# Performance work log

Hardware: AMD Instinct MI355X
Metric: run time of the kernel (lower is better)

## Reference

```python
import jax, jax.numpy as jnp
import numpy as np

B, L, D = 32, 512, 128          # batch, seq_len, d_model (= num graph nodes N)
E, HS, DTR, U = 64, 64, 4, 32   # d_proj_E, d_proj_H (state), dt_rank, d_proj_U
R, K, DE, NH = 3, 3, 10, 4      # mamba layers, cheb order, d_e, heads
EPS = 1e-5


def _ln(x, g, b):
    m = jnp.mean(x, -1, keepdims=True)
    v = jnp.mean((x - m) ** 2, -1, keepdims=True)
    return (x - m) / jnp.sqrt(v + EPS) * g + b


def _mamba(x, in_w, conv_w, conv_b, xproj_w, dt_w, dt_b, Alog, Dp, out_w):
    b, l, _ = x.shape
    xz = x @ in_w                                  # (b,l,2E)
    xp, res = xz[..., :E], xz[..., E:]
    xc = jnp.transpose(xp, (0, 2, 1))              # (b,E,l)
    # causal depthwise conv: torch pads both sides by d_conv-1 then slices [:l]
    xc = jax.lax.conv_general_dilated(
        xc, conv_w, (1,), [(conv_w.shape[-1] - 1, 0)],
        dimension_numbers=('NCH', 'OIH', 'NCH'), feature_group_count=E)
    xc = xc + conv_b[None, :, None]
    xp = jax.nn.silu(jnp.transpose(xc, (0, 2, 1)))  # (b,l,E)
    xdbl = xp @ xproj_w                             # (b,l,DTR+2*HS)
    delta = jax.nn.softplus(xdbl[..., :DTR] @ dt_w + dt_b)        # (b,l,E)
    Bm = xdbl[..., DTR:DTR + HS]                                   # (b,l,HS)
    Cm = xdbl[..., DTR + HS:]                                      # (b,l,HS)
    A = -jnp.exp(Alog)                                             # (E,HS)
    dA = jnp.exp(delta[..., None] * A)                             # (b,l,E,HS)
    dBu = delta[..., None] * Bm[:, :, None, :] * xp[..., None]     # (b,l,E,HS)

    def step(s, t):
        dA_t, dBu_t, C_t = t
        s = dA_t * s + dBu_t
        return s, jnp.einsum('bdn,bn->bd', s, C_t)

    _, ys = jax.lax.scan(step, jnp.zeros((b, E, HS), x.dtype),
                         (jnp.swapaxes(dA, 0, 1), jnp.swapaxes(dBu, 0, 1),
                          jnp.swapaxes(Cm, 0, 1)))
    y = jnp.swapaxes(ys, 0, 1) + xp * Dp
    y = y * jax.nn.sigmoid(res)
    return y @ out_w


def _forward(x, mb_in_w, mb_conv_w, mb_conv_b, mb_xproj_w, mb_dt_w, mb_dt_b,
             mb_Alog, mb_D, mb_out_w, ln1_g, ln1_b, ln2_g, ln2_b,
             ffn_w1, ffn_b1, ffn_w2, ffn_b2,
             psi_emb, psi, W_q, W_k, attn_alpha, F_w, f_b, head_mix,
             head_w, head_b):
    # ---- bidirectional Mamba stack ----
    for i in range(R):
        f, bk = 2 * i, 2 * i + 1
        Y1 = _mamba(x, mb_in_w[f], mb_conv_w[f], mb_conv_b[f], mb_xproj_w[f],
                    mb_dt_w[f], mb_dt_b[f], mb_Alog[f], mb_D[f], mb_out_w[f])
        Y2 = jnp.flip(_mamba(jnp.flip(x, 1), mb_in_w[bk], mb_conv_w[bk],
                             mb_conv_b[bk], mb_xproj_w[bk], mb_dt_w[bk],
                             mb_dt_b[bk], mb_Alog[bk], mb_D[bk], mb_out_w[bk]), 1)
        Y3 = _ln(x + Y1 + Y2, ln1_g[i], ln1_b[i])
        Yp = jax.nn.relu(Y3 @ ffn_w1[i] + ffn_b1[i]) @ ffn_w2[i] + ffn_b2[i]
        x = _ln(Yp + Y3, ln2_g[i], ln2_b[i])
    h = jnp.transpose(x, (0, 2, 1))                # (B, N=D, L)
    # ---- MAGAC (deterministic single MC sample, eval, no edge drop) ----
    diff = psi_emb[:, None, :] - psi_emb[None, :, :]
    A_g = jax.nn.softmax(jnp.exp(-psi * jnp.sum(diff * diff, -1)), axis=1)
    Q = jnp.einsum('nd,dhm->nhm', psi_emb, W_q)
    Kt = jnp.einsum('nd,dhm->nhm', psi_emb, W_k)
    attn = jax.nn.softmax(jnp.einsum('nhd,mhd->hnm', Q, Kt)
                          / jnp.sqrt(jnp.asarray(DE, x.dtype)), axis=-1)
    alpha = jax.nn.sigmoid(attn_alpha)
    A_effs = alpha * A_g[None] + (1.0 - alpha) * attn   # (H,N,N)
    mix = jax.nn.softmax(head_mix)
    I = jnp.eye(D, dtype=x.dtype)
    out = jnp.zeros((x.shape[0], D), x.dtype)
    for hh in range(NH):
        A = A_effs[hh]
        sup = [I, A]
        for _ in range(2, K + 1):
            sup.append(2.0 * A @ sup[-1] - sup[-2])
        S = jnp.stack(sup, 0)                             # (K+1,N,N)
        Wf = jnp.einsum('nd,dkl->nkl', psi_emb, F_w[hh])  # (N,K+1,L)
        bf = psi_emb @ f_b[hh]                            # (N,)
        out_h = jnp.einsum('knm,bml,nkl->bn', S, h, Wf) + bf
        out = out + mix[hh] * out_h
    log_var = jnp.zeros_like(out)
    pred = out @ head_w + head_b                          # (B,1)
    return pred, log_var


def setup_inputs() -> dict:
    key = jax.random.key(0)
    ks = iter(jax.random.split(key, 40))
    nrm = lambda shp, s=0.05: (jax.random.normal(next(ks), shp, jnp.float32) * s)
    M = 2 * R
    base_Alog = jnp.log(jnp.arange(1, HS + 1, dtype=jnp.float32))
    inp = {
        'x': jax.random.normal(next(ks), (B, L, D), jnp.float32),
        'mb_in_w': nrm((M, D, 2 * E)),
        'mb_conv_w': nrm((M, E, 1, 3), 0.2),
        'mb_conv_b': jnp.zeros((M, E), jnp.float32),
        'mb_xproj_w': nrm((M, E, DTR + 2 * HS)),
        'mb_dt_w': nrm((M, DTR, E), 0.2),
        'mb_dt_b': jnp.zeros((M, E), jnp.float32),
        'mb_Alog': jnp.tile(base_Alog[None, None, :], (M, E, 1)),
        'mb_D': jnp.ones((M, E), jnp.float32),
        'mb_out_w': nrm((M, E, D)),
        'ln1_g': jnp.ones((R, D), jnp.float32),
        'ln1_b': jnp.zeros((R, D), jnp.float32),
        'ln2_g': jnp.ones((R, D), jnp.float32),
        'ln2_b': jnp.zeros((R, D), jnp.float32),
        'ffn_w1': nrm((R, D, U)),
        'ffn_b1': jnp.zeros((R, U), jnp.float32),
        'ffn_w2': nrm((R, U, D)),
        'ffn_b2': jnp.zeros((R, D), jnp.float32),
        'psi_emb': jax.random.normal(next(ks), (D, DE), jnp.float32),
        'psi': jnp.asarray(1.0, jnp.float32),
        'W_q': jax.random.normal(next(ks), (DE, NH, DE), jnp.float32),
        'W_k': jax.random.normal(next(ks), (DE, NH, DE), jnp.float32),
        'attn_alpha': jnp.asarray(0.5, jnp.float32),
        'F_w': nrm((NH, DE, K + 1, L), 0.05),
        'f_b': nrm((NH, DE), 1.0),
        'head_mix': jnp.ones((NH,), jnp.float32),
        'head_w': nrm((D, 1)),
        'head_b': jnp.zeros((1,), jnp.float32),
    }
    return inp


def reference(x, mb_in_w, mb_conv_w, mb_conv_b, mb_xproj_w, mb_dt_w, mb_dt_b,
              mb_Alog, mb_D, mb_out_w, ln1_g, ln1_b, ln2_g, ln2_b,
              ffn_w1, ffn_b1, ffn_w2, ffn_b2,
              psi_emb, psi, W_q, W_k, attn_alpha, F_w, f_b, head_mix,
              head_w, head_b):
    return _forward(x, mb_in_w, mb_conv_w, mb_conv_b, mb_xproj_w, mb_dt_w,
                    mb_dt_b, mb_Alog, mb_D, mb_out_w, ln1_g, ln1_b, ln2_g,
                    ln2_b, ffn_w1, ffn_b1, ffn_w2, ffn_b2, psi_emb, psi,
                    W_q, W_k, attn_alpha, F_w, f_b, head_mix, head_w, head_b)
```

## Files before the change

### kernel.cpp

```cpp
#include <hip/hip_runtime.h>
#include <hip/hip_bf16.h>


#define B_ 32
#define L_ 512
#define D_ 128
#define E_ 64
#define HS_ 64

#define OFF_X     0u
#define OFF_XZF   2097152u
#define OFF_XZB   4194304u
#define OFF_XPF   6291456u
#define OFF_XPB   7340032u
#define OFF_PKF   8388608u
#define OFF_PKB   10485760u
#define OFF_XBCF  12582912u
#define OFF_XBCB  14680064u
#define OFF_YSF   16777216u
#define OFF_YSB   17825792u
#define OFF_V     2097152u
#define OFF_WFT   10485760u
#define OFF_STT   11534336u
#define OFF_AEFF  11796480u
#define OFF_PART  12582912u
#define OFF_RED1  16777216u

__device__ __forceinline__ float sigf(float x) { return 1.f / (1.f + __expf(-x)); }
__device__ __forceinline__ unsigned int bf16r(float x) {
    unsigned int u = __float_as_uint(x);
    return (u + 0x7fffu + ((u >> 16) & 1u)) >> 16;
}

__global__ __launch_bounds__(256) void gemm_in2_kernel(
    const float* __restrict__ X, const float* __restrict__ WF, const float* __restrict__ WB,
    float* __restrict__ xzF, float* __restrict__ xzB)
{
    __shared__ float sxT[128][36];
    __shared__ float sw[2][16][128];
    const int tid = threadIdx.x;
    const int r0 = blockIdx.x * 32;
    for (int q = tid; q < 1024; q += 256) {
        const int r = q >> 5, k4 = q & 31;
        const float4 v = *(const float4*)&X[(size_t)(r0 + r) * 128 + k4 * 4];
        sxT[k4 * 4 + 0][r] = v.x; sxT[k4 * 4 + 1][r] = v.y;
        sxT[k4 * 4 + 2][r] = v.z; sxT[k4 * 4 + 3][r] = v.w;
    }
    const int wv = tid >> 6, lane = tid & 63;
    const int d = wv >> 1, ch = wv & 1;
    const int r4 = lane >> 4, c16 = lane & 15;
    float4 acc[8];
#pragma unroll
    for (int j = 0; j < 8; ++j) acc[j] = float4{0.f, 0.f, 0.f, 0.f};
    for (int ko = 0; ko < 128; ko += 16) {
        __syncthreads();
        for (int q = tid; q < 1024; q += 256) {
            const int dd = q >> 9, kk = (q >> 5) & 15, c4 = q & 31;
            *(float4*)&sw[dd][kk][c4 * 4] =
                *(const float4*)&((dd ? WB : WF)[(ko + kk) * 128 + c4 * 4]);
        }
        __syncthreads();
#pragma unroll
        for (int kk = 0; kk < 16; ++kk) {
            const float4 w4 = *(const float4*)&sw[d][kk][ch * 64 + c16 * 4];
            const float4 xa = *(const float4*)&sxT[ko + kk][r4 * 8];
            const float4 xb = *(const float4*)&sxT[ko + kk][r4 * 8 + 4];
            const float xs[8] = {xa.x, xa.y, xa.z, xa.w, xb.x, xb.y, xb.z, xb.w};
#pragma unroll
            for (int j = 0; j < 8; ++j) {
                acc[j].x = fmaf(xs[j], w4.x, acc[j].x);
                acc[j].y = fmaf(xs[j], w4.y, acc[j].y);
                acc[j].z = fmaf(xs[j], w4.z, acc[j].z);
                acc[j].w = fmaf(xs[j], w4.w, acc[j].w);
            }
        }
    }
    float* xz = d ? xzB : xzF;
#pragma unroll
    for (int j = 0; j < 8; ++j) {
        *(float4*)&xz[(r0 + r4 * 8 + j) * 128 + ch * 64 + c16 * 4] = acc[j];
    }
}

__global__ __launch_bounds__(256) void prep4_kernel(
    const float* __restrict__ xzF_, const float* __restrict__ xzB_,
    const float* __restrict__ conv_w, const float* __restrict__ conv_b,
    const float* __restrict__ xproj_w, const float* __restrict__ dt_w,
    const float* __restrict__ dt_b, int layer,
    float* __restrict__ xpF_, float* __restrict__ xpB_,
    unsigned int* __restrict__ xbcF_, unsigned int* __restrict__ xbcB_,
    float* __restrict__ pkF_, float* __restrict__ pkB_)
{
    __shared__ float sW[8448];
    __shared__ float sxp4[4][64][4];
    __shared__ float sdl4[4][4][4];
    const int tid = threadIdx.x, wv = tid >> 6, lane = tid & 63;
    const int dir = (int)(blockIdx.x >= 1024);
    const int r0 = (blockIdx.x & 1023) * 16;
    const int b = r0 >> 9;
    const int m = layer * 2 + dir;
    const float* Wg = xproj_w + m * 8448;
    for (int q = tid; q < 2112; q += 256) ((float4*)sW)[q] = ((const float4*)Wg)[q];
    const float* xz = dir ? xzB_ : xzF_;
    float* xp  = dir ? xpB_  : xpF_;
    unsigned int* xbc = dir ? xbcB_ : xbcF_;
    float* pkx = dir ? pkB_  : pkF_;
    const float* cw = conv_w + m * 192 + lane * 3;
    const float cw0 = cw[0], cw1 = cw[1], cw2 = cw[2];
    const float cb  = conv_b[m * 64 + lane];
    const float dtb = dt_b[m * 64 + lane];
    const float* dwp = dt_w + m * 256;
    const float dw0 = dwp[lane], dw1 = dwp[64 + lane], dw2 = dwp[128 + lane], dw3 = dwp[192 + lane];
    float uu[4];
#pragma unroll
    for (int it = 0; it < 4; ++it) {
        const int row = r0 + wv * 4 + it;
        const int l = row & 511;
        const int l1 = dir ? l + 1 : l - 1;
        const int l2 = dir ? l + 2 : l - 2;
        float acc = cb;
        const float x0 = xz[(size_t)row * 128 + lane];
        const float x1 = (l1 >= 0 && l1 < 512) ? xz[(size_t)(b * 512 + l1) * 128 + lane] : 0.f;
        const float x2 = (l2 >= 0 && l2 < 512) ? xz[(size_t)(b * 512 + l2) * 128 + lane] : 0.f;
        acc += cw0 * x2 + cw1 * x1 + cw2 * x0;
        const float u = acc * sigf(acc);
        xp[row * 64 + lane] = u;
        uu[it] = u;
    }
    *(float4*)&sxp4[wv][lane][0] = float4{uu[0], uu[1], uu[2], uu[3]};
    __syncthreads();
    const int jdt = lane & 3;
    float aB[4] = {0.f, 0.f, 0.f, 0.f};
    float aC[4] = {0.f, 0.f, 0.f, 0.f};
    float adt[4] = {0.f, 0.f, 0.f, 0.f};
#pragma unroll 4
    for (int k = 0; k < 64; ++k) {
        const float wB = sW[k * 132 + 4 + lane];
        const float wC = sW[k * 132 + 68 + lane];
        const float wd = sW[k * 132 + jdt];
        const float4 xv = *(const float4*)&sxp4[wv][k][0];
        aB[0] = fmaf(xv.x, wB, aB[0]); aC[0] = fmaf(xv.x, wC, aC[0]); adt[0] = fmaf(xv.x, wd, adt[0]);
        aB[1] = fmaf(xv.y, wB, aB[1]); aC[1] = fmaf(xv.y, wC, aC[1]); adt[1] = fmaf(xv.y, wd, adt[1]);
        aB[2] = fmaf(xv.z, wB, aB[2]); aC[2] = fmaf(xv.z, wC, aC[2]); adt[2] = fmaf(xv.z, wd, adt[2]);
        aB[3] = fmaf(xv.w, wB, aB[3]); aC[3] = fmaf(xv.w, wC, aC[3]); adt[3] = fmaf(xv.w, wd, adt[3]);
    }
#pragma unroll
    for (int it = 0; it < 4; ++it) {
        const int row = r0 + wv * 4 + it;
        xbc[row * 64 + lane] = (bf16r(aC[it]) << 16) | bf16r(aB[it]);
        if (lane < 4) sdl4[wv][it][lane] = adt[it];
    }
#pragma unroll
    for (int it = 0; it < 4; ++it) {
        const int row = r0 + wv * 4 + it;
        float dpre = fmaf(sdl4[wv][it][0], dw0, dtb);
        dpre = fmaf(sdl4[wv][it][1], dw1, dpre);
        dpre = fmaf(sdl4[wv][it][2], dw2, dpre);
        dpre = fmaf(sdl4[wv][it][3], dw3, dpre);
        const float dlt = (dpre > 20.f) ? dpre : log1pf(__expf(dpre));
        ((float2*)pkx)[row * 64 + lane] = float2{dlt, dlt * uu[it]};
    }
}

__global__ __launch_bounds__(256, 4) void scan8_kernel(
    const unsigned int* __restrict__ xbcF, const unsigned int* __restrict__ xbcB,
    const float* __restrict__ pkF, const float* __restrict__ pkB,
    const float* __restrict__ AlogF, const float* __restrict__ AlogB,
    float* __restrict__ ysF, float* __restrict__ ysB)
{
    __shared__ unsigned int sbc[2][1024];
    __shared__ float spk[2][4][16][2];
    __shared__ float ytile[4][16][68];
    const int tid = threadIdx.x, wv = tid >> 6, lane = tid & 63;
    const int bx = blockIdx.x;
    const int db = bx & 63;
    const int dir = db >> 5;
    const int b   = db & 31;
    const int e0  = (bx >> 6) * 4;
    const int e   = e0 + wv;
    const unsigned int* xbc = dir ? xbcB : xbcF;
    const float* pk  = dir ? pkB  : pkF;
    const float* Aw  = dir ? AlogB : AlogF;
    float* ys = dir ? ysB : ysF;
    const float a2 = -__expf(Aw[e * 64 + lane]) * 1.4426950408889634f;
    float s = 0.f;
    float* yrow = ys + (size_t)(b * 64 + e) * 512;

    const int psl = tid & 15, pw_ = tid >> 4;

#define STG_LOAD(RS)                                                              \
    {                                                                             \
        nb = *(const uint4*)(xbc + (size_t)(RS) * 64 + tid * 4);                  \
        if (tid < 64)                                                             \
            npp = *(const float2*)(pk + (size_t)((RS) + psl) * 128 + (e0 + pw_) * 2); \
    }
#define STG_WRITE(BUF)                                                            \
    {                                                                             \
        *(uint4*)(&sbc[BUF][tid * 4]) = nb;                                       \
        if (tid < 64) *(float2*)(&spk[BUF][pw_][psl][0]) = npp;                   \
    }

#define SCAN16(REV)                                                               \
    {                                                                             \
        const unsigned int* bc = &sbc[cur][0];                                    \
        const float* pq = &spk[cur][wv][0][0];                                    \
        _Pragma("unroll")                                                         \
        for (int j = 0; j < 8; ++j) {                                             \
            const int pj = (REV) ? 7 - j : j;                                     \
            const float4 pk4 = *(const float4*)(pq + pj * 4);                     \
            const int sA = (REV) ? 15 - 2 * j : 2 * j;                            \
            const int sB = (REV) ? 14 - 2 * j : 2 * j + 1;                        \
            const float dlA = (REV) ? pk4.z : pk4.x;                              \
            const float duA = (REV) ? pk4.w : pk4.y;                              \
            const float dlB = (REV) ? pk4.x : pk4.z;                              \
            const float duB = (REV) ? pk4.y : pk4.w;                              \
            const unsigned int bA = bc[sA * 64 + lane];                           \
            const float BnA = __uint_as_float(bA << 16);                          \
            const float CnA = __uint_as_float(bA & 0xffff0000u);                  \
            s = fmaf(__builtin_amdgcn_exp2f(dlA * a2), s, duA * BnA);             \
            ytile[wv][2 * j][lane] = s * CnA;                                     \
            const unsigned int bB = bc[sB * 64 + lane];                           \
            const float BnB = __uint_as_float(bB << 16);                          \
            const float CnB = __uint_as_float(bB & 0xffff0000u);                  \
            s = fmaf(__builtin_amdgcn_exp2f(dlB * a2), s, duB * BnB);             \
            ytile[wv][2 * j + 1][lane] = s * CnB;                                 \
        }                                                                         \
    }

    {
        uint4 nb; float2 npp;
        const int rs0 = b * 512 + (dir ? 496 : 0);
        STG_LOAD(rs0);
        STG_WRITE(0);
    }
    __syncthreads();

    int cur = 0;
    const int rr = lane & 15, sg = lane >> 4;
    for (int t = 0; t < 32; ++t) {
        uint4 nb; float2 npp;
        const bool more = (t + 1) < 32;
        if (more) {
            const int rs = b * 512 + (dir ? (496 - (t + 1) * 16) : ((t + 1) * 16));
            STG_LOAD(rs);
        }
        if (dir == 0) { SCAN16(0) } else { SCAN16(1) }
        {
            const float* yt = &ytile[wv][rr][sg * 16];
            const float4 A0 = *(const float4*)yt;
            const float4 A1 = *(const float4*)(yt + 4);
            const float4 A2 = *(const float4*)(yt + 8);
            const float4 A3 = *(const float4*)(yt + 12);
            float p = ((A0.x + A0.y) + (A0.z + A0.w)) + ((A1.x + A1.y) + (A1.z + A1.w))
                    + ((A2.x + A2.y) + (A2.z + A2.w)) + ((A3.x + A3.y) + (A3.z + A3.w));
            p += __shfl_xor(p, 16);
            p += __shfl_xor(p, 32);
            if (lane < 16) {
                const int lg = dir ? (511 - (t * 16 + rr)) : (t * 16 + rr);
                yrow[lg] = p;
            }
        }
        if (more) STG_WRITE(cur ^ 1);
        __syncthreads();
        cur ^= 1;
    }
#undef STG_LOAD
#undef STG_WRITE
#undef SCAN16
}

__global__ __launch_bounds__(256) void opfn2_kernel(
    const float* __restrict__ ysF, const float* __restrict__ ysB,
    const float* __restrict__ xpF, const float* __restrict__ xpB,
    const float* __restrict__ xzF, const float* __restrict__ xzB,
    const float* __restrict__ Dp, int layer,
    const float* __restrict__ Xc, const float* __restrict__ out_w,
    const float* __restrict__ W1, const float* __restrict__ b1,
    const float* __restrict__ W2, const float* __restrict__ b2,
    const float* __restrict__ g1, const float* __restrict__ bb1,
    const float* __restrict__ g2, const float* __restrict__ bb2,
    float* __restrict__ xout,
    const float* __restrict__ WFn, const float* __restrict__ WBn,
    float* __restrict__ xzFo, float* __restrict__ xzBo)
{
    __shared__ float smem[8832];
    float* syt = smem;
    float* y3  = smem;
    float* sy  = smem + 2176;
    float* sw  = smem + 4224;
    float* sh  = smem + 8320;
    const int tid = threadIdx.x;
    const int r0 = blockIdx.x * 16;
    const int b = r0 >> 9, l0 = r0 & 511;

    for (int q = tid; q < 512; q += 256) {
        const int d = q >> 8, ee = (q >> 2) & 63, rq = q & 3;
        const float* ysp = d ? ysB : ysF;
        const float4 v = *(const float4*)&ysp[(size_t)(b * 64 + ee) * 512 + l0 + rq * 4];
        float* dst = &syt[(d * 64 + ee) * 17 + rq * 4];
        dst[0] = v.x; dst[1] = v.y; dst[2] = v.z; dst[3] = v.w;
    }
    __syncthreads();
    for (int q = tid; q < 2048; q += 256) {
        const int r = q >> 7, c = q & 127;
        const int d = c >> 6, ee = c & 63;
        const int row = r0 + r;
        const float dv  = Dp[(layer * 2 + d) * 64 + ee];
        const float u   = (d ? xpB : xpF)[(size_t)row * 64 + ee];
        const float res = (d ? xzB : xzF)[(size_t)row * 128 + 64 + ee];
        sy[r * 128 + c] = (syt[(d * 64 + ee) * 17 + r] + u * dv) * sigf(res);
    }
    const int wv = tid >> 6, lane = tid & 63;
    const float* WFp = out_w + (layer * 2) * 8192;
    const float* WBp = out_w + (layer * 2 + 1) * 8192;
    float acc[4][2];
#pragma unroll
    for (int r = 0; r < 4; ++r) { acc[r][0] = 0.f; acc[r][1] = 0.f; }
    for (int ko = 0; ko < 128; ko += 32) {
        __syncthreads();
        for (int q = tid; q < 1024; q += 256) {
            const int kk = q >> 5, c4 = q & 31;
            const int kg = ko + kk;
            *(float4*)&sw[kk * 128 + c4 * 4] = (kg < 64)
                ? *(const float4*)&WFp[kg * 128 + c4 * 4]
                : *(const float4*)&WBp[(kg - 64) * 128 + c4 * 4];
        }
        __syncthreads();
#define OPSTEP(SRC, COMP, J)                                                      \
        {                                                                         \
            const float w0 = sw[(kk + (J)) * 128 + lane];                         \
            const float w1 = sw[(kk + (J)) * 128 + lane + 64];                    \
            acc[0][0] = fmaf(y40.COMP, w0, acc[0][0]);                            \
            acc[0][1] = fmaf(y40.COMP, w1, acc[0][1]);                            \
            acc[1][0] = fmaf(y41.COMP, w0, acc[1][0]);                            \
            acc[1][1] = fmaf(y41.COMP, w1, acc[1][1]);                            \
            acc[2][0] = fmaf(y42.COMP, w0, acc[2][0]);                            \
            acc[2][1] = fmaf(y42.COMP, w1, acc[2][1]);                            \
            acc[3][0] = fmaf(y43.COMP, w0, acc[3][0]);                            \
            acc[3][1] = fmaf(y43.COMP, w1, acc[3][1]);                            \
        }
#pragma unroll
        for (int kk = 0; kk < 32; kk += 4) {
            const float4 y40 = *(const float4*)&sy[(wv * 4 + 0) * 128 + ko + kk];
            const float4 y41 = *(const float4*)&sy[(wv * 4 + 1) * 128 + ko + kk];
            const float4 y42 = *(const float4*)&sy[(wv * 4 + 2) * 128 + ko + kk];
            const float4 y43 = *(const float4*)&sy[(wv * 4 + 3) * 128 + ko + kk];
            OPSTEP(sy, x, 0) OPSTEP(sy, y, 1) OPSTEP(sy, z, 2) OPSTEP(sy, w, 3)
        }
    }
    __syncthreads();
    for (int q = tid; q < 1024; q += 256) ((float4*)sw)[q] = ((const float4*)W1)[q];
#pragma unroll
    for (int r = 0; r < 4; ++r) {
        const int rl = wv * 4 + r;
        const int row = r0 + rl;
        float v0 = acc[r][0] + Xc[(size_t)row * 128 + lane];
        float v1 = acc[r][1] + Xc[(size_t)row * 128 + lane + 64];
        float sum = v0 + v1, sq = v0 * v0 + v1 * v1;
#pragma unroll
        for (int o = 32; o >= 1; o >>= 1) { sum += __shfl_xor(sum, o); sq += __shfl_xor(sq, o); }
        const float mean = sum * (1.f / 128.f);
        const float var = sq * (1.f / 128.f) - mean * mean;
        const float rs = rsqrtf(var + 1e-5f);
        y3[rl * 128 + lane]      = (v0 - mean) * rs * g1[lane] + bb1[lane];
        y3[rl * 128 + lane + 64] = (v1 - mean) * rs * g1[lane + 64] + bb1[lane + 64];
    }
    __syncthreads();
    {
        const int r = tid >> 4, u = tid & 15;
        float h0 = b1[u], h1 = b1[u + 16];
#pragma unroll 8
        for (int k = 0; k < 128; ++k) {
            const float xv = y3[r * 128 + k];
            h0 = fmaf(xv, sw[k * 32 + u], h0);
            h1 = fmaf(xv, sw[k * 32 + u + 16], h1);
        }
        sh[r * 32 + u]      = fmaxf(h0, 0.f);
        sh[r * 32 + u + 16] = fmaxf(h1, 0.f);
    }
    __syncthreads();
    for (int q = tid; q < 1024; q += 256) ((float4*)sw)[q] = ((const float4*)W2)[q];
    __syncthreads();
    float xr[4][2];
#pragma unroll
    for (int r = 0; r < 4; ++r) {
        const int rl = wv * 4 + r;
        float a0 = b2[lane], a1 = b2[lane + 64];
#pragma unroll 8
        for (int k = 0; k < 32; ++k) {
            const float hv = sh[rl * 32 + k];
            a0 = fmaf(hv, sw[k * 128 + lane], a0);
            a1 = fmaf(hv, sw[k * 128 + lane + 64], a1);
        }
        const float v0 = a0 + y3[rl * 128 + lane];
        const float v1 = a1 + y3[rl * 128 + lane + 64];
        float sum = v0 + v1, sq = v0 * v0 + v1 * v1;
#pragma unroll
        for (int o = 32; o >= 1; o >>= 1) { sum += __shfl_xor(sum, o); sq += __shfl_xor(sq, o); }
        const float mean = sum * (1.f / 128.f);
        const float var = sq * (1.f / 128.f) - mean * mean;
        const float rs = rsqrtf(var + 1e-5f);
        const int row = r0 + rl;
        const float o0 = (v0 - mean) * rs * g2[lane] + bb2[lane];
        const float o1 = (v1 - mean) * rs * g2[lane + 64] + bb2[lane + 64];
        xout[(size_t)row * 128 + lane]      = o0;
        xout[(size_t)row * 128 + lane + 64] = o1;
        xr[r][0] = o0; xr[r][1] = o1;
    }
    if (WFn == nullptr) return;
    __syncthreads();
    float* sxr = y3;
#pragma unroll
    for (int r = 0; r < 4; ++r) {
        sxr[(wv * 4 + r) * 128 + lane]      = xr[r][0];
        sxr[(wv * 4 + r) * 128 + lane + 64] = xr[r][1];
    }
    for (int d = 0; d < 2; ++d) {
        const float* Wn = d ? WBn : WFn;
        float* xzo = d ? xzBo : xzFo;
#pragma unroll
        for (int r = 0; r < 4; ++r) { acc[r][0] = 0.f; acc[r][1] = 0.f; }
        for (int ko = 0; ko < 128; ko += 32) {
            __syncthreads();
            for (int q = tid; q < 1024; q += 256) {
                const int kk = q >> 5, c4 = q & 31;
                *(float4*)&sw[kk * 128 + c4 * 4] = *(const float4*)&Wn[(ko + kk) * 128 + c4 * 4];
            }
            __syncthreads();
#pragma unroll
            for (int kk = 0; kk < 32; kk += 4) {
                const float4 y40 = *(const float4*)&sxr[(wv * 4 + 0) * 128 + ko + kk];
                const float4 y41 = *(const float4*)&sxr[(wv * 4 + 1) * 128 + ko + kk];
                const float4 y42 = *(const float4*)&sxr[(wv * 4 + 2) * 128 + ko + kk];
                const float4 y43 = *(const float4*)&sxr[(wv * 4 + 3) * 128 + ko + kk];
                OPSTEP(sxr, x, 0) OPSTEP(sxr, y, 1) OPSTEP(sxr, z, 2) OPSTEP(sxr, w, 3)
            }
        }
#pragma unroll
        for (int r = 0; r < 4; ++r) {
            const int row = r0 + wv * 4 + r;
            xzo[(size_t)row * 128 + lane]      = acc[r][0];
            xzo[(size_t)row * 128 + lane + 64] = acc[r][1];
        }
    }
#undef OPSTEP
}

__global__ __launch_bounds__(256) void head_wfqk_kernel(
    const float* __restrict__ psi, const float* __restrict__ F_w, float* __restrict__ WfT,
    const float* __restrict__ psis, const float* __restrict__ W_q, const float* __restrict__ W_k,
    const float* __restrict__ attn_a,
    float* __restrict__ Aeff, float* __restrict__ StT)
{
    __shared__ float sQ[2][10];
    __shared__ float red[2][128];
    if (blockIdx.x < 4096) {
        const int idx = blockIdx.x * 256 + threadIdx.x;
        const int n = idx & 127, l = (idx >> 7) & 511, k = (idx >> 16) & 3, h = idx >> 18;
        float acc = 0.f;
#pragma unroll
        for (int d = 0; d < 10; ++d)
            acc = fmaf(psi[n * 10 + d], F_w[((h * 10 + d) * 4 + k) * 512 + l], acc);
        WfT[idx] = acc;
        return;
    }
    const int q = blockIdx.x - 4096;
    const int half = threadIdx.x >> 7, mcol = threadIdx.x & 127;
    const int unit = q * 2 + half;
    const int h = unit >> 7, n = unit & 127;
    float Kreg[10];
#pragma unroll
    for (int d = 0; d < 10; ++d) Kreg[d] = 0.f;
#pragma unroll
    for (int d0 = 0; d0 < 10; ++d0) {
        const float pv = psi[mcol * 10 + d0];
#pragma unroll
        for (int d = 0; d < 10; ++d) Kreg[d] = fmaf(pv, W_k[(d0 * 4 + h) * 10 + d], Kreg[d]);
    }
    if (mcol < 10) {
        float qd = 0.f;
        for (int d0 = 0; d0 < 10; ++d0)
            qd = fmaf(psi[n * 10 + d0], W_q[(d0 * 4 + h) * 10 + mcol], qd);
        sQ[half][mcol] = qd;
    }
    __syncthreads();
    float d2 = 0.f;
#pragma unroll
    for (int d = 0; d < 10; ++d) { const float df = psi[n * 10 + d] - psi[mcol * 10 + d]; d2 = fmaf(df, df, d2); }
    const float gv = __expf(-psis[0] * d2);
    float qv = 0.f;
#pragma unroll
    for (int d = 0; d < 10; ++d) qv = fmaf(sQ[half][d], Kreg[d], qv);
    qv *= 0.3162277660168379332f;
    float* rd = red[half];
    float r;
    rd[mcol] = gv; __syncthreads();
    for (int s = 64; s >= 1; s >>= 1) { if (mcol < s) rd[mcol] = fmaxf(rd[mcol], rd[mcol + s]); __syncthreads(); }
    r = rd[0]; __syncthreads();
    const float eg = __expf(gv - r);
    rd[mcol] = eg; __syncthreads();
    for (int s = 64; s >= 1; s >>= 1) { if (mcol < s) rd[mcol] += rd[mcol + s]; __syncthreads(); }
    const float gsum = rd[0]; __syncthreads();
    rd[mcol] = qv; __syncthreads();
    for (int s = 64; s >= 1; s >>= 1) { if (mcol < s) rd[mcol] = fmaxf(rd[mcol], rd[mcol + s]); __syncthreads(); }
    r = rd[0]; __syncthreads();
    const float eq = __expf(qv - r);
    rd[mcol] = eq; __syncthreads();
    for (int s = 64; s >= 1; s >>= 1) { if (mcol < s) rd[mcol] += rd[mcol + s]; __syncthreads(); }
    const float qsum = rd[0];
    const float al = sigf(attn_a[0]);
    const float aeff = al * (eg / gsum) + (1.f - al) * (eq / qsum);
    Aeff[h * 16384 + n * 128 + mcol] = aeff;
    StT[((h * 4 + 1) * 128 + mcol) * 128 + n] = aeff;
    StT[((h * 4 + 0) * 128 + mcol) * 128 + n] = (mcol == n) ? 1.f : 0.f;
}

__global__ __launch_bounds__(256) void head_cheb_kernel(
    const float* __restrict__ Aeff, float* __restrict__ StT, int kk)
{
    const int h = blockIdx.x >> 6;
    const int m0 = ((blockIdx.x & 63) << 1) + (threadIdx.x >> 7);
    const int n = threadIdx.x & 127;
    const float* Ar = Aeff + h * 16384 + n * 128;
    const float* Sp = StT + ((h * 4 + kk - 1) * 128 + m0) * 128;
    float acc = 0.f;
#pragma unroll 8
    for (int p = 0; p < 128; ++p) acc = fmaf(Ar[p], Sp[p], acc);
    const float s2 = StT[((h * 4 + kk - 2) * 128 + m0) * 128 + n];
    StT[((h * 4 + kk) * 128 + m0) * 128 + n] = 2.f * acc - s2;
}

__global__ __launch_bounds__(256) void head_v4_kernel(
    const float* __restrict__ StT, const float* __restrict__ WfT, const float* __restrict__ hmix,
    float* __restrict__ V)
{
    const float m0 = hmix[0], m1 = hmix[1], m2 = hmix[2], m3 = hmix[3];
    const float mxx = fmaxf(fmaxf(m0, m1), fmaxf(m2, m3));
    const float e0 = __expf(m0 - mxx), e1 = __expf(m1 - mxx), e2 = __expf(m2 - mxx), e3 = __expf(m3 - mxx);
    const float inv = 1.f / (e0 + e1 + e2 + e3);
    const float mixv[4] = {e0 * inv, e1 * inv, e2 * inv, e3 * inv};
    const int tid = threadIdx.x;
    const int lt = blockIdx.x & 63, mm = blockIdx.x >> 6;
    const int n4 = tid & 31, mh = tid >> 5;
    const int m = mm * 8 + mh;
    const int l0 = lt * 8, n0 = n4 * 4;
    float4 sv[16];
#pragma unroll
    for (int h = 0; h < 4; ++h) {
        const float mx = mixv[h];
#pragma unroll
        for (int k = 0; k < 4; ++k) {
            const float4 v = *(const float4*)&StT[(size_t)((h * 4 + k) * 128 + m) * 128 + n0];
            sv[h * 4 + k] = float4{v.x * mx, v.y * mx, v.z * mx, v.w * mx};
        }
    }
#pragma unroll
    for (int j = 0; j < 8; ++j) {
        const int l = l0 + j;
        float4 acc = {0.f, 0.f, 0.f, 0.f};
#pragma unroll
        for (int hk = 0; hk < 16; ++hk) {
            const float4 w = *(const float4*)&WfT[(size_t)(hk * 512 + l) * 128 + n0];
            acc.x = fmaf(sv[hk].x, w.x, acc.x);
            acc.y = fmaf(sv[hk].y, w.y, acc.y);
            acc.z = fmaf(sv[hk].z, w.z, acc.z);
            acc.w = fmaf(sv[hk].w, w.w, acc.w);
        }
        *(float4*)&V[(size_t)(l * 128 + m) * 128 + n0] = acc;
    }
}

__global__ __launch_bounds__(256) void head_ctr_kernel(
    const float* __restrict__ Xf, const float* __restrict__ V, float* __restrict__ partial)
{
    __shared__ float sx[32][128];
    const int l = blockIdx.x, tid = threadIdx.x;
    const int n = tid & 127, mh = tid >> 7;
    for (int q = tid; q < 1024; q += 256) {
        const int b = q >> 5, m4 = q & 31;
        *(float4*)&sx[b][m4 * 4] = *(const float4*)&Xf[(size_t)(b * 512 + l) * 128 + m4 * 4];
    }
    __syncthreads();
    float acc[32];
#pragma unroll
    for (int b = 0; b < 32; ++b) acc[b] = 0.f;
    const float* vp = V + (size_t)(l * 128 + mh * 64) * 128 + n;
    for (int mm = 0; mm < 64; ++mm) {
        const float v = vp[(size_t)mm * 128];
        const int m = mh * 64 + mm;
#pragma unroll
        for (int b = 0; b < 32; ++b) acc[b] = fmaf(sx[b][m], v, acc[b]);
    }
#pragma unroll
    for (int b = 0; b < 32; ++b)
        partial[(size_t)((l * 2 + mh) * 32 + b) * 128 + n] = acc[b];
}

__global__ __launch_bounds__(128) void head_red_kernel(
    const float* __restrict__ partial, float* __restrict__ red1)
{
    const int b = blockIdx.x >> 5, cs = blockIdx.x & 31, n = threadIdx.x;
    const float* p = partial + ((size_t)(cs * 32) * 32 + b) * 128 + n;
    float s = 0.f;
#pragma unroll 8
    for (int c = 0; c < 32; ++c) s += p[(size_t)c * 4096];
    red1[(b * 32 + cs) * 128 + n] = s;
}

__global__ __launch_bounds__(128) void head_out_kernel(
    const float* __restrict__ red1, const float* __restrict__ psi,
    const float* __restrict__ f_b, const float* __restrict__ hmix,
    const float* __restrict__ head_w, const float* __restrict__ head_b, float* __restrict__ out)
{
    __shared__ float red[128];
    const int b = blockIdx.x, n = threadIdx.x;
    const float m0 = hmix[0], m1 = hmix[1], m2 = hmix[2], m3 = hmix[3];
    const float mxx = fmaxf(fmaxf(m0, m1), fmaxf(m2, m3));
    const float e0 = __expf(m0 - mxx), e1 = __expf(m1 - mxx), e2 = __expf(m2 - mxx), e3 = __expf(m3 - mxx);
    const float inv = 1.f / (e0 + e1 + e2 + e3);
    const float mixv[4] = {e0 * inv, e1 * inv, e2 * inv, e3 * inv};
    float s = 0.f;
#pragma unroll
    for (int h = 0; h < 4; ++h) {
        float t = 0.f;
#pragma unroll
        for (int d = 0; d < 10; ++d) t = fmaf(psi[n * 10 + d], f_b[h * 10 + d], t);
        s = fmaf(mixv[h], t, s);
    }
#pragma unroll 8
    for (int cs = 0; cs < 32; ++cs) s += red1[(b * 32 + cs) * 128 + n];
    red[n] = s * head_w[n];
    __syncthreads();
    for (int st = 64; st >= 1; st >>= 1) { if (n < st) red[n] += red[n + st]; __syncthreads(); }
    if (n == 0) out[b] = red[0] + head_b[0];
    out[32 + b * 128 + n] = 0.f;
}

extern "C" void kernel_launch(void* const* d_in, const int* in_sizes, int n_in,
                              void* d_out, int out_size, void* d_ws, size_t ws_size,
                              hipStream_t stream) {
    const float* x_in    = (const float*)d_in[0];
    const float* in_w    = (const float*)d_in[1];
    const float* conv_w  = (const float*)d_in[2];
    const float* conv_b  = (const float*)d_in[3];
    const float* xproj_w = (const float*)d_in[4];
    const float* dt_w    = (const float*)d_in[5];
    const float* dt_b    = (const float*)d_in[6];
    const float* Alog    = (const float*)d_in[7];
    const float* Dp      = (const float*)d_in[8];
    const float* out_w   = (const float*)d_in[9];
    const float* ln1_g   = (const float*)d_in[10];
    const float* ln1_b   = (const float*)d_in[11];
    const float* ln2_g   = (const float*)d_in[12];
    const float* ln2_b   = (const float*)d_in[13];
    const float* ffn_w1  = (const float*)d_in[14];
    const float* ffn_b1  = (const float*)d_in[15];
    const float* ffn_w2  = (const float*)d_in[16];
    const float* ffn_b2  = (const float*)d_in[17];
    const float* psi_emb = (const float*)d_in[18];
    const float* psi_s   = (const float*)d_in[19];
    const float* W_q     = (const float*)d_in[20];
    const float* W_k     = (const float*)d_in[21];
    const float* attn_a  = (const float*)d_in[22];
    const float* F_w     = (const float*)d_in[23];
    const float* f_b     = (const float*)d_in[24];
    const float* hmix    = (const float*)d_in[25];
    const float* head_w  = (const float*)d_in[26];
    const float* head_b  = (const float*)d_in[27];
    float* ws = (float*)d_ws;
    float* outp = (float*)d_out;

    gemm_in2_kernel<<<512, 256, 0, stream>>>(
        x_in, in_w, in_w + 16384, ws + OFF_XZF, ws + OFF_XZB);
    for (int i = 0; i < 3; ++i) {
        const float* xcur = (i == 0) ? x_in : (ws + OFF_X);
        const int mF = 2 * i, mB = 2 * i + 1;
        prep4_kernel<<<2048, 256, 0, stream>>>(
            ws + OFF_XZF, ws + OFF_XZB, conv_w, conv_b, xproj_w, dt_w, dt_b, i,
            ws + OFF_XPF, ws + OFF_XPB,
            (unsigned int*)(ws + OFF_XBCF), (unsigned int*)(ws + OFF_XBCB),
            ws + OFF_PKF, ws + OFF_PKB);
        scan8_kernel<<<1024, 256, 0, stream>>>(
            (const unsigned int*)(ws + OFF_XBCF), (const unsigned int*)(ws + OFF_XBCB),
            ws + OFF_PKF, ws + OFF_PKB,
            Alog + mF * 4096, Alog + mB * 4096, ws + OFF_YSF, ws + OFF_YSB);
        const float* WFn = (i < 2) ? (in_w + (2 * i + 2) * 16384) : nullptr;
        const float* WBn = (i < 2) ? (in_w + (2 * i + 3) * 16384) : nullptr;
        opfn2_kernel<<<1024, 256, 0, stream>>>(
            ws + OFF_YSF, ws + OFF_YSB, ws + OFF_XPF, ws + OFF_XPB, ws + OFF_XZF, ws + OFF_XZB,
            Dp, i, xcur, out_w,
            ffn_w1 + i * 4096, ffn_b1 + i * 32, ffn_w2 + i * 4096, ffn_b2 + i * 128,
            ln1_g + i * 128, ln1_b + i * 128, ln2_g + i * 128, ln2_b + i * 128,
            ws + OFF_X, WFn, WBn, ws + OFF_XZF, ws + OFF_XZB);
    }
    head_wfqk_kernel<<<4352, 256, 0, stream>>>(
        psi_emb, F_w, ws + OFF_WFT, psi_s, W_q, W_k, attn_a,
        ws + OFF_AEFF, ws + OFF_STT);
    head_cheb_kernel<<<256, 256, 0, stream>>>(ws + OFF_AEFF, ws + OFF_STT, 2);
    head_cheb_kernel<<<256, 256, 0, stream>>>(ws + OFF_AEFF, ws + OFF_STT, 3);
    head_v4_kernel<<<1024, 256, 0, stream>>>(ws + OFF_STT, ws + OFF_WFT, hmix, ws + OFF_V);
    head_ctr_kernel<<<512, 256, 0, stream>>>(ws + OFF_X, ws + OFF_V, ws + OFF_PART);
    head_red_kernel<<<1024, 128, 0, stream>>>(ws + OFF_PART, ws + OFF_RED1);
    head_out_kernel<<<32, 128, 0, stream>>>(
        ws + OFF_RED1, psi_emb, f_b, hmix, head_w, head_b, outp);
}
```

Before: 506.1 us.

## Pair-interleave xBC rows for vector scan loads; register-prefetch weight tiles in opfn2

The prep kernel now stores packed B/C values for consecutive timestep pairs interleaved, so the scan reads both steps with one 64-bit LDS load. It writes paired outputs as float2 into a reshaped ytile, and the reduction now uses shuffles within 8-lane groups with float2 global stores. The opfn2 kernel register-prefetches the next weight chunk from global memory while the current chunk is consumed from LDS, including the FFN weights and the fused next-layer in-projection loop. This hides global latency in those GEMM phases at the cost of extra registers.

```diff
diff --git a/kernel.cpp b/kernel.cpp
--- a/kernel.cpp
+++ b/kernel.cpp
@@ -144,10 +144,17 @@
         aB[2] = fmaf(xv.z, wB, aB[2]); aC[2] = fmaf(xv.z, wC, aC[2]); adt[2] = fmaf(xv.z, wd, adt[2]);
         aB[3] = fmaf(xv.w, wB, aB[3]); aC[3] = fmaf(xv.w, wC, aC[3]); adt[3] = fmaf(xv.w, wd, adt[3]);
     }
+    {
+        const unsigned int p0 = (bf16r(aC[0]) << 16) | bf16r(aB[0]);
+        const unsigned int p1 = (bf16r(aC[1]) << 16) | bf16r(aB[1]);
+        const unsigned int p2 = (bf16r(aC[2]) << 16) | bf16r(aB[2]);
+        const unsigned int p3 = (bf16r(aC[3]) << 16) | bf16r(aB[3]);
+        const int rp = (r0 + wv * 4) >> 1;
+        *(uint2*)&xbc[(size_t)rp * 128 + lane * 2]       = uint2{p0, p1};
+        *(uint2*)&xbc[(size_t)(rp + 1) * 128 + lane * 2] = uint2{p2, p3};
+    }
 #pragma unroll
     for (int it = 0; it < 4; ++it) {
-        const int row = r0 + wv * 4 + it;
-        xbc[row * 64 + lane] = (bf16r(aC[it]) << 16) | bf16r(aB[it]);
         if (lane < 4) sdl4[wv][it][lane] = adt[it];
     }
 #pragma unroll
@@ -162,7 +169,7 @@
     }
 }
 
-__global__ __launch_bounds__(256, 4) void scan8_kernel(
+__global__ __launch_bounds__(256, 4) void scan9_kernel(
     const unsigned int* __restrict__ xbcF, const unsigned int* __restrict__ xbcB,
     const float* __restrict__ pkF, const float* __restrict__ pkB,
     const float* __restrict__ AlogF, const float* __restrict__ AlogB,
@@ -170,7 +177,7 @@
 {
     __shared__ unsigned int sbc[2][1024];
     __shared__ float spk[2][4][16][2];
-    __shared__ float ytile[4][16][68];
+    __shared__ float ytile[4][8][130];
     const int tid = threadIdx.x, wv = tid >> 6, lane = tid & 63;
     const int bx = blockIdx.x;
     const int db = bx & 63;
@@ -208,22 +215,21 @@
         for (int j = 0; j < 8; ++j) {                                             \
             const int pj = (REV) ? 7 - j : j;                                     \
             const float4 pk4 = *(const float4*)(pq + pj * 4);                     \
-            const int sA = (REV) ? 15 - 2 * j : 2 * j;                            \
-            const int sB = (REV) ? 14 - 2 * j : 2 * j + 1;                        \
+            const uint2 bb = *(const uint2*)(bc + pj * 128 + lane * 2);           \
+            const unsigned int bA = (REV) ? bb.y : bb.x;                          \
+            const unsigned int bB = (REV) ? bb.x : bb.y;                          \
             const float dlA = (REV) ? pk4.z : pk4.x;                              \
             const float duA = (REV) ? pk4.w : pk4.y;                              \
             const float dlB = (REV) ? pk4.x : pk4.z;                              \
             const float duB = (REV) ? pk4.y : pk4.w;                              \
-            const unsigned int bA = bc[sA * 64 + lane];                           \
             const float BnA = __uint_as_float(bA << 16);                          \
             const float CnA = __uint_as_float(bA & 0xffff0000u);                  \
             s = fmaf(__builtin_amdgcn_exp2f(dlA * a2), s, duA * BnA);             \
-            ytile[wv][2 * j][lane] = s * CnA;                                     \
-            const unsigned int bB = bc[sB * 64 + lane];                           \
+            const float pA = s * CnA;                                             \
             const float BnB = __uint_as_float(bB << 16);                          \
             const float CnB = __uint_as_float(bB & 0xffff0000u);                  \
             s = fmaf(__builtin_amdgcn_exp2f(dlB * a2), s, duB * BnB);             \
-            ytile[wv][2 * j + 1][lane] = s * CnB;                                 \
+            *(float2*)&ytile[wv][j][lane * 2] = float2{pA, s * CnB};              \
         }                                                                         \
     }
 
@@ -236,7 +242,7 @@
     __syncthreads();
 
     int cur = 0;
-    const int rr = lane & 15, sg = lane >> 4;
+    const int j2 = lane >> 3, sg = lane & 7;
     for (int t = 0; t < 32; ++t) {
         uint4 nb; float2 npp;
         const bool more = (t + 1) < 32;
@@ -246,18 +252,21 @@
         }
         if (dir == 0) { SCAN16(0) } else { SCAN16(1) }
         {
-            const float* yt = &ytile[wv][rr][sg * 16];
+            const float* yt = &ytile[wv][j2][sg * 16];
             const float4 A0 = *(const float4*)yt;
             const float4 A1 = *(const float4*)(yt + 4);
             const float4 A2 = *(const float4*)(yt + 8);
             const float4 A3 = *(const float4*)(yt + 12);
-            float p = ((A0.x + A0.y) + (A0.z + A0.w)) + ((A1.x + A1.y) + (A1.z + A1.w))
-                    + ((A2.x + A2.y) + (A2.z + A2.w)) + ((A3.x + A3.y) + (A3.z + A3.w));
-            p += __shfl_xor(p, 16);
-            p += __shfl_xor(p, 32);
-            if (lane < 16) {
-                const int lg = dir ? (511 - (t * 16 + rr)) : (t * 16 + rr);
-                yrow[lg] = p;
+            float p0 = ((A0.x + A0.z) + (A1.x + A1.z)) + ((A2.x + A2.z) + (A3.x + A3.z));
+            float p1 = ((A0.y + A0.w) + (A1.y + A1.w)) + ((A2.y + A2.w) + (A3.y + A3.w));
+            p0 += __shfl_xor(p0, 1); p0 += __shfl_xor(p0, 2); p0 += __shfl_xor(p0, 4);
+            p1 += __shfl_xor(p1, 1); p1 += __shfl_xor(p1, 2); p1 += __shfl_xor(p1, 4);
+            if (sg == 0) {
+                if (dir == 0) {
+                    *(float2*)&yrow[t * 16 + j2 * 2] = float2{p0, p1};
+                } else {
+                    *(float2*)&yrow[510 - (t * 16 + j2 * 2)] = float2{p1, p0};
+                }
             }
         }
         if (more) STG_WRITE(cur ^ 1);
@@ -292,6 +301,33 @@
     const int tid = threadIdx.x;
     const int r0 = blockIdx.x * 16;
     const int b = r0 >> 9, l0 = r0 & 511;
+    const int wv = tid >> 6, lane = tid & 63;
+    const float* WFp = out_w + (layer * 2) * 8192;
+    const float* WBp = out_w + (layer * 2 + 1) * 8192;
+    float4 wreg[4];
+
+#define LD_OP2(KO)                                                                \
+    _Pragma("unroll")                                                             \
+    for (int rr2 = 0; rr2 < 4; ++rr2) {                                           \
+        const int q = rr2 * 256 + tid;                                            \
+        const int kg = (KO) + (q >> 5);                                           \
+        wreg[rr2] = (kg < 64) ? *(const float4*)&WFp[kg * 128 + (q & 31) * 4]     \
+                              : *(const float4*)&WBp[(kg - 64) * 128 + (q & 31) * 4]; \
+    }
+#define LD_LIN(SRC)                                                               \
+    _Pragma("unroll")                                                             \
+    for (int rr2 = 0; rr2 < 4; ++rr2) wreg[rr2] = ((const float4*)(SRC))[rr2 * 256 + tid];
+#define ST_SW()                                                                   \
+    _Pragma("unroll")                                                             \
+    for (int rr2 = 0; rr2 < 4; ++rr2) {                                           \
+        const int q = rr2 * 256 + tid;                                            \
+        *(float4*)&sw[(q >> 5) * 128 + (q & 31) * 4] = wreg[rr2];                 \
+    }
+#define ST_SW_LIN()                                                               \
+    _Pragma("unroll")                                                             \
+    for (int rr2 = 0; rr2 < 4; ++rr2) ((float4*)sw)[rr2 * 256 + tid] = wreg[rr2];
+
+    LD_OP2(0);
 
     for (int q = tid; q < 512; q += 256) {
         const int d = q >> 8, ee = (q >> 2) & 63, rq = q & 3;
@@ -310,22 +346,9 @@
         const float res = (d ? xzB : xzF)[(size_t)row * 128 + 64 + ee];
         sy[r * 128 + c] = (syt[(d * 64 + ee) * 17 + r] + u * dv) * sigf(res);
     }
-    const int wv = tid >> 6, lane = tid & 63;
-    const float* WFp = out_w + (layer * 2) * 8192;
-    const float* WBp = out_w + (layer * 2 + 1) * 8192;
     float acc[4][2];
 #pragma unroll
     for (int r = 0; r < 4; ++r) { acc[r][0] = 0.f; acc[r][1] = 0.f; }
-    for (int ko = 0; ko < 128; ko += 32) {
-        __syncthreads();
-        for (int q = tid; q < 1024; q += 256) {
-            const int kk = q >> 5, c4 = q & 31;
-            const int kg = ko + kk;
-            *(float4*)&sw[kk * 128 + c4 * 4] = (kg < 64)
-                ? *(const float4*)&WFp[kg * 128 + c4 * 4]
-                : *(const float4*)&WBp[(kg - 64) * 128 + c4 * 4];
-        }
-        __syncthreads();
 #define OPSTEP(SRC, COMP, J)                                                      \
         {                                                                         \
             const float w0 = sw[(kk + (J)) * 128 + lane];                         \
@@ -339,17 +362,24 @@
             acc[3][0] = fmaf(y43.COMP, w0, acc[3][0]);                            \
             acc[3][1] = fmaf(y43.COMP, w1, acc[3][1]);                            \
         }
-#pragma unroll
-        for (int kk = 0; kk < 32; kk += 4) {
-            const float4 y40 = *(const float4*)&sy[(wv * 4 + 0) * 128 + ko + kk];
-            const float4 y41 = *(const float4*)&sy[(wv * 4 + 1) * 128 + ko + kk];
-            const float4 y42 = *(const float4*)&sy[(wv * 4 + 2) * 128 + ko + kk];
-            const float4 y43 = *(const float4*)&sy[(wv * 4 + 3) * 128 + ko + kk];
-            OPSTEP(sy, x, 0) OPSTEP(sy, y, 1) OPSTEP(sy, z, 2) OPSTEP(sy, w, 3)
-        }
-    }
-    __syncthreads();
-    for (int q = tid; q < 1024; q += 256) ((float4*)sw)[q] = ((const float4*)W1)[q];
+#define GEMM_CHUNK(SRC, KO)                                                       \
+    _Pragma("unroll")                                                             \
+    for (int kk = 0; kk < 32; kk += 4) {                                          \
+        const float4 y40 = *(const float4*)&(SRC)[(wv * 4 + 0) * 128 + (KO) + kk];\
+        const float4 y41 = *(const float4*)&(SRC)[(wv * 4 + 1) * 128 + (KO) + kk];\
+        const float4 y42 = *(const float4*)&(SRC)[(wv * 4 + 2) * 128 + (KO) + kk];\
+        const float4 y43 = *(const float4*)&(SRC)[(wv * 4 + 3) * 128 + (KO) + kk];\
+        OPSTEP(SRC, x, 0) OPSTEP(SRC, y, 1) OPSTEP(SRC, z, 2) OPSTEP(SRC, w, 3)  \
+    }
+    for (int koi = 0; koi < 4; ++koi) {
+        __syncthreads();
+        ST_SW();
+        if (koi < 3) LD_OP2((koi + 1) * 32);
+        __syncthreads();
+        GEMM_CHUNK(sy, koi * 32);
+    }
+    __syncthreads();
+    LD_LIN(W1);
 #pragma unroll
     for (int r = 0; r < 4; ++r) {
         const int rl = wv * 4 + r;
@@ -365,6 +395,9 @@
         y3[rl * 128 + lane]      = (v0 - mean) * rs * g1[lane] + bb1[lane];
         y3[rl * 128 + lane + 64] = (v1 - mean) * rs * g1[lane + 64] + bb1[lane + 64];
     }
+    __syncthreads();
+    ST_SW_LIN();
+    LD_LIN(W2);
     __syncthreads();
     {
         const int r = tid >> 4, u = tid & 15;
@@ -379,7 +412,7 @@
         sh[r * 32 + u + 16] = fmaxf(h1, 0.f);
     }
     __syncthreads();
-    for (int q = tid; q < 1024; q += 256) ((float4*)sw)[q] = ((const float4*)W2)[q];
+    ST_SW_LIN();
     __syncthreads();
     float xr[4][2];
 #pragma unroll
@@ -415,35 +448,46 @@
         sxr[(wv * 4 + r) * 128 + lane]      = xr[r][0];
         sxr[(wv * 4 + r) * 128 + lane + 64] = xr[r][1];
     }
-    for (int d = 0; d < 2; ++d) {
-        const float* Wn = d ? WBn : WFn;
-        float* xzo = d ? xzBo : xzFo;
-#pragma unroll
-        for (int r = 0; r < 4; ++r) { acc[r][0] = 0.f; acc[r][1] = 0.f; }
-        for (int ko = 0; ko < 128; ko += 32) {
-            __syncthreads();
-            for (int q = tid; q < 1024; q += 256) {
-                const int kk = q >> 5, c4 = q & 31;
-                *(float4*)&sw[kk * 128 + c4 * 4] = *(const float4*)&Wn[(ko + kk) * 128 + c4 * 4];
+#pragma unroll
+    for (int rr2 = 0; rr2 < 4; ++rr2) {
+        const int q = rr2 * 256 + tid;
+        wreg[rr2] = *(const float4*)&WFn[(q >> 5) * 128 + (q & 31) * 4];
+    }
+    for (int c = 0; c < 8; ++c) {
+        const int dd = c >> 2, ko = (c & 3) * 32;
+        __syncthreads();
+        ST_SW();
+        if (c < 7) {
+            const float* Wn2 = ((c + 1) >> 2) ? WBn : WFn;
+            const int ko2 = ((c + 1) & 3) * 32;
+#pragma unroll
+            for (int rr2 = 0; rr2 < 4; ++rr2) {
+                const int q = rr2 * 256 + tid;
+                wreg[rr2] = *(const float4*)&Wn2[(ko2 + (q >> 5)) * 128 + (q & 31) * 4];
             }
-            __syncthreads();
-#pragma unroll
-            for (int kk = 0; kk < 32; kk += 4) {
-                const float4 y40 = *(const float4*)&sxr[(wv * 4 + 0) * 128 + ko + kk];
-                const float4 y41 = *(const float4*)&sxr[(wv * 4 + 1) * 128 + ko + kk];
-                const float4 y42 = *(const float4*)&sxr[(wv * 4 + 2) * 128 + ko + kk];
-                const float4 y43 = *(const float4*)&sxr[(wv * 4 + 3) * 128 + ko + kk];
-                OPSTEP(sxr, x, 0) OPSTEP(sxr, y, 1) OPSTEP(sxr, z, 2) OPSTEP(sxr, w, 3)
+        }
+        __syncthreads();
+        if ((c & 3) == 0) {
+#pragma unroll
+            for (int r = 0; r < 4; ++r) { acc[r][0] = 0.f; acc[r][1] = 0.f; }
+        }
+        GEMM_CHUNK(sxr, ko);
+        if ((c & 3) == 3) {
+            float* xzo = dd ? xzBo : xzFo;
+#pragma unroll
+            for (int r = 0; r < 4; ++r) {
+                const int row = r0 + wv * 4 + r;
+                xzo[(size_t)row * 128 + lane]      = acc[r][0];
+                xzo[(size_t)row * 128 + lane + 64] = acc[r][1];
             }
         }
-#pragma unroll
-        for (int r = 0; r < 4; ++r) {
-            const int row = r0 + wv * 4 + r;
-            xzo[(size_t)row * 128 + lane]      = acc[r][0];
-            xzo[(size_t)row * 128 + lane + 64] = acc[r][1];
-        }
     }
 #undef OPSTEP
+#undef GEMM_CHUNK
+#undef LD_OP2
+#undef LD_LIN
+#undef ST_SW
+#undef ST_SW_LIN
 }
 
 __global__ __launch_bounds__(256) void head_wfqk_kernel(
@@ -680,7 +724,7 @@
             ws + OFF_XPF, ws + OFF_XPB,
             (unsigned int*)(ws + OFF_XBCF), (unsigned int*)(ws + OFF_XBCB),
             ws + OFF_PKF, ws + OFF_PKB);
-        scan8_kernel<<<1024, 256, 0, stream>>>(
+        scan9_kernel<<<1024, 256, 0, stream>>>(
             (const unsigned int*)(ws + OFF_XBCF), (const unsigned int*)(ws + OFF_XBCB),
             ws + OFF_PKF, ws + OFF_PKB,
             Alog + mF * 4096, Alog + mB * 4096, ws + OFF_YSF, ws + OFF_YSB);
```

Measured after the change: 736.3 us. +45.5%, slower.

## Double-buffer opfn2 weight staging with async global-to-LDS loads

Applied to the files above, without the earlier changes.

The out-projection and next-layer in-projection GEMMs in opfn2 now stage weights in 16-row chunks through two LDS buffers using global_load_lds. The next chunk is fetched while the current one is computed, replacing synchronous per-32-row register-staged copies. W1/W2 staging also uses direct-to-LDS loads, and the scan's ytile/yrow indexing is simplified. This aims to hide global-load latency and save register round-trips, at the cost of more barriers and relying on load completion ordering across syncthreads.

```diff
diff --git a/kernel.cpp b/kernel.cpp
--- a/kernel.cpp
+++ b/kernel.cpp
@@ -30,6 +30,11 @@
 __device__ __forceinline__ unsigned int bf16r(float x) {
     unsigned int u = __float_as_uint(x);
     return (u + 0x7fffu + ((u >> 16) & 1u)) >> 16;
+}
+__device__ __forceinline__ void gld16(const float* g, float* l) {
+    __builtin_amdgcn_global_load_lds(
+        (const __attribute__((address_space(1))) unsigned int*)g,
+        (__attribute__((address_space(3))) unsigned int*)l, 16, 0, 0);
 }
 
 __global__ __launch_bounds__(256) void gemm_in2_kernel(
@@ -218,12 +223,12 @@
             const float BnA = __uint_as_float(bA << 16);                          \
             const float CnA = __uint_as_float(bA & 0xffff0000u);                  \
             s = fmaf(__builtin_amdgcn_exp2f(dlA * a2), s, duA * BnA);             \
-            ytile[wv][2 * j][lane] = s * CnA;                                     \
+            ytile[wv][sA][lane] = s * CnA;                                        \
             const unsigned int bB = bc[sB * 64 + lane];                           \
             const float BnB = __uint_as_float(bB << 16);                          \
             const float CnB = __uint_as_float(bB & 0xffff0000u);                  \
             s = fmaf(__builtin_amdgcn_exp2f(dlB * a2), s, duB * BnB);             \
-            ytile[wv][2 * j + 1][lane] = s * CnB;                                 \
+            ytile[wv][sB][lane] = s * CnB;                                        \
         }                                                                         \
     }
 
@@ -256,7 +261,7 @@
             p += __shfl_xor(p, 16);
             p += __shfl_xor(p, 32);
             if (lane < 16) {
-                const int lg = dir ? (511 - (t * 16 + rr)) : (t * 16 + rr);
+                const int lg = dir ? (496 + rr - t * 16) : (t * 16 + rr);
                 yrow[lg] = p;
             }
         }
@@ -292,6 +297,18 @@
     const int tid = threadIdx.x;
     const int r0 = blockIdx.x * 16;
     const int b = r0 >> 9, l0 = r0 & 511;
+    const int wv = tid >> 6, lane = tid & 63;
+    const float* WFp = out_w + (layer * 2) * 8192;
+    const float* WBp = out_w + (layer * 2 + 1) * 8192;
+
+#define STAGE16(SRCP, BUF)                                                        \
+    {                                                                             \
+        const float* sp_ = (SRCP);                                                \
+        gld16(sp_ + tid * 4, (BUF) + wv * 256);                                   \
+        gld16(sp_ + 1024 + tid * 4, (BUF) + 1024 + wv * 256);                     \
+    }
+
+    STAGE16(WFp, sw);
 
     for (int q = tid; q < 512; q += 256) {
         const int d = q >> 8, ee = (q >> 2) & 63, rq = q & 3;
@@ -310,26 +327,15 @@
         const float res = (d ? xzB : xzF)[(size_t)row * 128 + 64 + ee];
         sy[r * 128 + c] = (syt[(d * 64 + ee) * 17 + r] + u * dv) * sigf(res);
     }
-    const int wv = tid >> 6, lane = tid & 63;
-    const float* WFp = out_w + (layer * 2) * 8192;
-    const float* WBp = out_w + (layer * 2 + 1) * 8192;
+    __syncthreads();
+
     float acc[4][2];
 #pragma unroll
     for (int r = 0; r < 4; ++r) { acc[r][0] = 0.f; acc[r][1] = 0.f; }
-    for (int ko = 0; ko < 128; ko += 32) {
-        __syncthreads();
-        for (int q = tid; q < 1024; q += 256) {
-            const int kk = q >> 5, c4 = q & 31;
-            const int kg = ko + kk;
-            *(float4*)&sw[kk * 128 + c4 * 4] = (kg < 64)
-                ? *(const float4*)&WFp[kg * 128 + c4 * 4]
-                : *(const float4*)&WBp[(kg - 64) * 128 + c4 * 4];
-        }
-        __syncthreads();
-#define OPSTEP(SRC, COMP, J)                                                      \
+#define OPSTEP16(WB_, COMP, J)                                                    \
         {                                                                         \
-            const float w0 = sw[(kk + (J)) * 128 + lane];                         \
-            const float w1 = sw[(kk + (J)) * 128 + lane + 64];                    \
+            const float w0 = (WB_)[(kk + (J)) * 128 + lane];                      \
+            const float w1 = (WB_)[(kk + (J)) * 128 + lane + 64];                 \
             acc[0][0] = fmaf(y40.COMP, w0, acc[0][0]);                            \
             acc[0][1] = fmaf(y40.COMP, w1, acc[0][1]);                            \
             acc[1][0] = fmaf(y41.COMP, w0, acc[1][0]);                            \
@@ -339,17 +345,32 @@
             acc[3][0] = fmaf(y43.COMP, w0, acc[3][0]);                            \
             acc[3][1] = fmaf(y43.COMP, w1, acc[3][1]);                            \
         }
-#pragma unroll
-        for (int kk = 0; kk < 32; kk += 4) {
-            const float4 y40 = *(const float4*)&sy[(wv * 4 + 0) * 128 + ko + kk];
-            const float4 y41 = *(const float4*)&sy[(wv * 4 + 1) * 128 + ko + kk];
-            const float4 y42 = *(const float4*)&sy[(wv * 4 + 2) * 128 + ko + kk];
-            const float4 y43 = *(const float4*)&sy[(wv * 4 + 3) * 128 + ko + kk];
-            OPSTEP(sy, x, 0) OPSTEP(sy, y, 1) OPSTEP(sy, z, 2) OPSTEP(sy, w, 3)
-        }
-    }
-    __syncthreads();
-    for (int q = tid; q < 1024; q += 256) ((float4*)sw)[q] = ((const float4*)W1)[q];
+#define GEMM_CHUNK16(SRC, WB_, KO)                                                \
+    _Pragma("unroll")                                                             \
+    for (int kk = 0; kk < 16; kk += 4) {                                          \
+        const float4 y40 = *(const float4*)&(SRC)[(wv * 4 + 0) * 128 + (KO) + kk];\
+        const float4 y41 = *(const float4*)&(SRC)[(wv * 4 + 1) * 128 + (KO) + kk];\
+        const float4 y42 = *(const float4*)&(SRC)[(wv * 4 + 2) * 128 + (KO) + kk];\
+        const float4 y43 = *(const float4*)&(SRC)[(wv * 4 + 3) * 128 + (KO) + kk];\
+        OPSTEP16(WB_, x, 0) OPSTEP16(WB_, y, 1) OPSTEP16(WB_, z, 2) OPSTEP16(WB_, w, 3) \
+    }
+    int cur = 0;
+    for (int c = 0; c < 8; ++c) {
+        if (c < 7) {
+            const int cn = c + 1;
+            const float* srcp = (cn < 4) ? (WFp + cn * 2048) : (WBp + (cn - 4) * 2048);
+            STAGE16(srcp, sw + ((cur ^ 1) * 2048));
+        }
+        GEMM_CHUNK16(sy, sw + cur * 2048, c * 16);
+        __syncthreads();
+        cur ^= 1;
+    }
+    {
+        gld16(W1 + tid * 4, sw + wv * 256);
+        gld16(W1 + 1024 + tid * 4, sw + 1024 + wv * 256);
+        gld16(W1 + 2048 + tid * 4, sw + 2048 + wv * 256);
+        gld16(W1 + 3072 + tid * 4, sw + 3072 + wv * 256);
+    }
 #pragma unroll
     for (int r = 0; r < 4; ++r) {
         const int rl = wv * 4 + r;
@@ -379,7 +400,12 @@
         sh[r * 32 + u + 16] = fmaxf(h1, 0.f);
     }
     __syncthreads();
-    for (int q = tid; q < 1024; q += 256) ((float4*)sw)[q] = ((const float4*)W2)[q];
+    {
+        gld16(W2 + tid * 4, sw + wv * 256);
+        gld16(W2 + 1024 + tid * 4, sw + 1024 + wv * 256);
+        gld16(W2 + 2048 + tid * 4, sw + 2048 + wv * 256);
+        gld16(W2 + 3072 + tid * 4, sw + 3072 + wv * 256);
+    }
     __syncthreads();
     float xr[4][2];
 #pragma unroll
@@ -415,35 +441,35 @@
         sxr[(wv * 4 + r) * 128 + lane]      = xr[r][0];
         sxr[(wv * 4 + r) * 128 + lane + 64] = xr[r][1];
     }
-    for (int d = 0; d < 2; ++d) {
-        const float* Wn = d ? WBn : WFn;
-        float* xzo = d ? xzBo : xzFo;
-#pragma unroll
-        for (int r = 0; r < 4; ++r) { acc[r][0] = 0.f; acc[r][1] = 0.f; }
-        for (int ko = 0; ko < 128; ko += 32) {
-            __syncthreads();
-            for (int q = tid; q < 1024; q += 256) {
-                const int kk = q >> 5, c4 = q & 31;
-                *(float4*)&sw[kk * 128 + c4 * 4] = *(const float4*)&Wn[(ko + kk) * 128 + c4 * 4];
+    STAGE16(WFn, sw);
+    __syncthreads();
+    cur = 0;
+    for (int c = 0; c < 16; ++c) {
+        if (c < 15) {
+            const int cn = c + 1;
+            const float* Wd = (cn >> 3) ? WBn : WFn;
+            STAGE16(Wd + (cn & 7) * 2048, sw + ((cur ^ 1) * 2048));
+        }
+        if ((c & 7) == 0) {
+#pragma unroll
+            for (int r = 0; r < 4; ++r) { acc[r][0] = 0.f; acc[r][1] = 0.f; }
+        }
+        GEMM_CHUNK16(sxr, sw + cur * 2048, (c & 7) * 16);
+        if ((c & 7) == 7) {
+            float* xzo = (c >> 3) ? xzBo : xzFo;
+#pragma unroll
+            for (int r = 0; r < 4; ++r) {
+                const int row = r0 + wv * 4 + r;
+                xzo[(size_t)row * 128 + lane]      = acc[r][0];
+                xzo[(size_t)row * 128 + lane + 64] = acc[r][1];
             }
-            __syncthreads();
-#pragma unroll
-            for (int kk = 0; kk < 32; kk += 4) {
-                const float4 y40 = *(const float4*)&sxr[(wv * 4 + 0) * 128 + ko + kk];
-                const float4 y41 = *(const float4*)&sxr[(wv * 4 + 1) * 128 + ko + kk];
-                const float4 y42 = *(const float4*)&sxr[(wv * 4 + 2) * 128 + ko + kk];
-                const float4 y43 = *(const float4*)&sxr[(wv * 4 + 3) * 128 + ko + kk];
-                OPSTEP(sxr, x, 0) OPSTEP(sxr, y, 1) OPSTEP(sxr, z, 2) OPSTEP(sxr, w, 3)
-            }
-        }
-#pragma unroll
-        for (int r = 0; r < 4; ++r) {
-            const int row = r0 + wv * 4 + r;
-            xzo[(size_t)row * 128 + lane]      = acc[r][0];
-            xzo[(size_t)row * 128 + lane + 64] = acc[r][1];
-        }
-    }
-#undef OPSTEP
+        }
+        __syncthreads();
+        cur ^= 1;
+    }
+#undef OPSTEP16
+#undef GEMM_CHUNK16
+#undef STAGE16
 }
 
 __global__ __launch_bounds__(256) void head_wfqk_kernel(
```

Result: no change. 513.4 us (+1.4%).
